# Performance work log

Measured on AMD Instinct MI355X. Metric: run time of the kernel, lower is better.

The kernel has to match this reference:

```python
import jax, jax.numpy as jnp
import numpy as np

jax.config.update("jax_enable_x64", True)  # original uses complex128 FFTs

MS_H, MS_W, MS_D = 10, 10, 2
EPS = 1e-08


def _window_mean(x, wx, wy, wz):
    """Mean over all (wx,wy,wz) VALID windows of 3D x, via a summed-area table.
    Equivalent math to tf.nn.avg_pool3d(stride 1, VALID)."""
    X, Y, Z = x.shape
    A, B, C = X - wx + 1, Y - wy + 1, Z - wz + 1  # (2*MS_W+1, 2*MS_H+1, 2*MS_D+1)
    S = jnp.pad(jnp.cumsum(jnp.cumsum(jnp.cumsum(x, 0), 1), 2), ((1, 0), (1, 0), (1, 0)))
    g = lambda ox, oy, oz: jax.lax.dynamic_slice(S, (ox, oy, oz), (A, B, C))
    ws = (g(wx, wy, wz) - g(0, wy, wz) - g(wx, 0, wz) - g(wx, wy, 0)
          + g(0, 0, wz) + g(0, wy, 0) + g(wx, 0, 0) - g(0, 0, 0))
    return ws / float(wx * wy * wz)


def _forward(fr, template):
    # fr: (1, X, Y, Z, 1) float32; template: (X, Y, Z, 1) float32
    tpl = template[..., 0]                       # (X, Y, Z)
    X, Y, Z = tpl.shape
    # --- normalize_template ---
    tpl_zm = tpl - jnp.mean(tpl)
    tpl_var = jnp.sum(jnp.square(tpl_zm)) + EPS  # scalar
    target_freq = jnp.fft.fftn(tpl_zm.astype(jnp.complex128), axes=(0, 1, 2))
    # --- normalize_image ---
    img = fr[0, ..., 0]                          # (X, Y, Z)
    imgs_zm = img - jnp.mean(img)
    wx, wy, wz = X - 2 * MS_W, Y - 2 * MS_H, Z - 2 * MS_D
    m1 = _window_mean(img, wx, wy, wz)           # avg_pool3d of img
    m2 = _window_mean(jnp.square(img), wx, wy, wz)
    shp_prod = float(X * Y * Z)
    imgs_var = m2 - jnp.square(m1) / shp_prod + EPS
    imgs_var = jnp.where(imgs_var < 0, jnp.zeros_like(imgs_var), imgs_var)
    denominator = jnp.sqrt(tpl_var * imgs_var)   # (21, 21, 5)
    # --- FFT cross-correlation ---
    fr_freq = jnp.fft.fftn(imgs_zm.astype(jnp.complex128), axes=(0, 1, 2))
    cc = jnp.abs(jnp.fft.ifftn(fr_freq * jnp.conj(target_freq), axes=(0, 1, 2))).astype(jnp.float32)
    mx, my, mz = X // 2, Y // 2, Z // 2
    rolled_cc = jnp.roll(cc, (mx, my, mz), axis=(0, 1, 2))
    ncc = rolled_cc[mx - MS_W:mx + MS_W + 1,
                    my - MS_H:my + MS_H + 1,
                    mz - MS_D:mz + MS_D + 1] / denominator.astype(jnp.float32)
    ncc = jnp.where(jnp.isnan(ncc), jnp.zeros_like(ncc), ncc)
    # --- argmax_3d + Gaussian subpixel refine ---
    A, B, C = ncc.shape
    flat_idx = jnp.argmax(ncc.reshape(-1))
    sx = flat_idx // (B * C)
    sy = (flat_idx % (B * C)) // C
    sz = flat_idx - sx * (B * C) - C * sy
    ncc_log = jnp.log(ncc)
    v = lambda dx, dy, dz: ncc_log[sx + dx, sy + dy, sz + dz]
    six = 6.0 * v(0, 0, 0)
    sh_x = (-(sx - MS_H)).astype(jnp.float32) - (v(-1, 0, 0) - v(1, 0, 0)) / (2 * v(-1, 0, 0) - six + 2 * v(1, 0, 0))
    sh_y = (-(sy - MS_W)).astype(jnp.float32) - (v(0, -1, 0) - v(0, 1, 0)) / (2 * v(0, -1, 0) - six + 2 * v(0, 1, 0))
    sh_z = (-(sz - MS_D)).astype(jnp.float32) - (v(0, 0, -1) - v(0, 0, 1)) / (2 * v(0, 0, -1) - six + 2 * v(0, 0, 1))
    return (sh_x.reshape(1, 1), sh_y.reshape(1, 1), sh_z.reshape(1, 1),
            rolled_cc[None, ..., None], ncc[None, ..., None])


def setup_inputs() -> dict:
    key = jax.random.key(0)
    k1, k2 = jax.random.split(key)
    X, Y, Z = 512, 512, 32
    base = jax.random.normal(k1, (X, Y, Z), dtype=jnp.float32)
    # box-smooth so the NCC has a broad positive peak (log-interp stays finite)
    sm = base
    for ax in range(3):
        sm = sum(jnp.roll(sm, s, ax) for s in (-2, -1, 0, 1, 2)) / 5.0
    template = sm[..., None]
    fr = (jnp.roll(sm, (3, -2, 1), axis=(0, 1, 2))
          + 0.02 * jax.random.normal(k2, (X, Y, Z), dtype=jnp.float32))[None, ..., None]
    return {"fr": fr, "template": template}


def reference(fr, template):
    return _forward(fr, template)
```

## Files before the change

### kernel.cpp

```cpp
#include <hip/hip_runtime.h>
#include <hip/hip_bf16.h>
#include <math.h>


#define NTOT 8388608
#define NLINES 262144
#define OUT_ROLL_OFF 3
#define OUT_NCC_OFF 8388611
#define WIN_PROD 6777792.0
#define EPSV 1e-8

#define WS_HC_OFF 0UL
#define WS_ZS1_OFF 67108864UL
#define WS_ZS2_OFF 77594624UL
#define WS_YS1_OFF 88080384UL
#define WS_YS2_OFF 88510464UL
#define WS_PART_OFF 88940544UL
#define WS_DENOM_OFF 88957952UL

typedef float2 cf;
__device__ __forceinline__ cf cfadd(cf a, cf b){ return make_float2(a.x+b.x, a.y+b.y); }
__device__ __forceinline__ cf cfsub(cf a, cf b){ return make_float2(a.x-b.x, a.y-b.y); }
__device__ __forceinline__ cf cfmul(cf a, cf b){ return make_float2(a.x*b.x-a.y*b.y, a.x*b.y+a.y*b.x); }
__device__ __forceinline__ cf cfnegi(cf a){ return make_float2(a.y, -a.x); }
__device__ __forceinline__ cf cfposi(cf a){ return make_float2(-a.y, a.x); }

#define RT2F 0.70710678118654752440f
__device__ __forceinline__ cf cw64f(cf v){ return make_float2(RT2F*(v.x+v.y), RT2F*(v.y-v.x)); }
__device__ __forceinline__ cf cw192f(cf v){ return make_float2(RT2F*(v.y-v.x), -RT2F*(v.x+v.y)); }
__device__ __forceinline__ cf cw64i(cf v){ return make_float2(RT2F*(v.x-v.y), RT2F*(v.x+v.y)); }
__device__ __forceinline__ cf cw192i(cf v){ return make_float2(-RT2F*(v.x+v.y), RT2F*(v.x-v.y)); }

#define SKW(i) ((i) + ((i) >> 3))
#define LROW 580

template <int H>
__device__ __forceinline__ void fwd_r4(cf* ln, const cf* tw, int lane) {
    const int MUL2 = 256 / (2 * H);
#pragma unroll
    for (int g = 0; g < 2; ++g) {
        int j = lane + 64 * g;
        int t = j & (H - 1);
        int i0 = ((j & ~(H - 1)) << 2) + t;
        cf A = ln[SKW(i0)];
        cf B = ln[SKW(i0 + H)];
        cf C = ln[SKW(i0 + 2 * H)];
        cf D = ln[SKW(i0 + 3 * H)];
        cf w1 = tw[t * MUL2];
        cf w2 = make_float2(w1.x * w1.x - w1.y * w1.y, 2.0f * w1.x * w1.y);
        cf u = cfadd(A, C), v = cfadd(B, D);
        cf p = cfmul(cfsub(A, C), w1);
        cf q = cfnegi(cfmul(cfsub(B, D), w1));
        ln[SKW(i0)]         = cfadd(u, v);
        ln[SKW(i0 + H)]     = cfmul(cfsub(u, v), w2);
        ln[SKW(i0 + 2 * H)] = cfadd(p, q);
        ln[SKW(i0 + 3 * H)] = cfmul(cfsub(p, q), w2);
    }
}

template <int H>
__device__ __forceinline__ void inv_r4(cf* ln, const cf* tw, int lane) {
    const int MUL2 = 256 / (2 * H);
#pragma unroll
    for (int g = 0; g < 2; ++g) {
        int j = lane + 64 * g;
        int t = j & (H - 1);
        int i0 = ((j & ~(H - 1)) << 2) + t;
        cf A = ln[SKW(i0)];
        cf B = ln[SKW(i0 + H)];
        cf C = ln[SKW(i0 + 2 * H)];
        cf D = ln[SKW(i0 + 3 * H)];
        cf tww = tw[t * MUL2];
        cf w2 = make_float2(tww.x, -tww.y);
        cf wH = make_float2(w2.x * w2.x - w2.y * w2.y, 2.0f * w2.x * w2.y);
        cf vb = cfmul(B, wH), vd = cfmul(D, wH);
        cf a0 = cfadd(A, vb), a1 = cfsub(A, vb);
        cf c0 = cfadd(C, vd), c1 = cfsub(C, vd);
        cf t0 = cfmul(c0, w2);
        cf t1 = cfposi(cfmul(c1, w2));
        ln[SKW(i0)]         = cfadd(a0, t0);
        ln[SKW(i0 + 2 * H)] = cfsub(a0, t0);
        ln[SKW(i0 + H)]     = cfadd(a1, t1);
        ln[SKW(i0 + 3 * H)] = cfsub(a1, t1);
    }
}

__device__ __forceinline__ void fwd_r8(cf* ln, int lane) {
    cf* rp = ln + 9 * lane;
    cf L0 = rp[0], L1 = rp[1], L2 = rp[2], L3 = rp[3];
    cf L4 = rp[4], L5 = rp[5], L6 = rp[6], L7 = rp[7];
    cf s0 = cfadd(L0, L4), d0 = cfsub(L0, L4);
    cf s1 = cfadd(L1, L5), d1 = cw64f(cfsub(L1, L5));
    cf s2 = cfadd(L2, L6), d2 = cfnegi(cfsub(L2, L6));
    cf s3 = cfadd(L3, L7), d3 = cw192f(cfsub(L3, L7));
    cf e0 = cfadd(s0, s2), e2 = cfsub(s0, s2);
    cf e1 = cfadd(s1, s3), e3 = cfnegi(cfsub(s1, s3));
    cf f0 = cfadd(d0, d2), f2 = cfsub(d0, d2);
    cf f1 = cfadd(d1, d3), f3 = cfnegi(cfsub(d1, d3));
    rp[0] = cfadd(e0, e1); rp[1] = cfsub(e0, e1);
    rp[2] = cfadd(e2, e3); rp[3] = cfsub(e2, e3);
    rp[4] = cfadd(f0, f1); rp[5] = cfsub(f0, f1);
    rp[6] = cfadd(f2, f3); rp[7] = cfsub(f2, f3);
}

__device__ __forceinline__ void inv_r8(cf* ln, int lane) {
    cf* rp = ln + 9 * lane;
    cf L0 = rp[0], L1 = rp[1], L2 = rp[2], L3 = rp[3];
    cf L4 = rp[4], L5 = rp[5], L6 = rp[6], L7 = rp[7];
    cf a0 = cfadd(L0, L1), a1 = cfsub(L0, L1), a2 = cfadd(L2, L3), a3 = cfsub(L2, L3);
    cf a4 = cfadd(L4, L5), a5 = cfsub(L4, L5), a6 = cfadd(L6, L7), a7 = cfsub(L6, L7);
    cf b0 = cfadd(a0, a2), b2 = cfsub(a0, a2);
    cf v13 = cfposi(a3);
    cf b1 = cfadd(a1, v13), b3 = cfsub(a1, v13);
    cf b4 = cfadd(a4, a6), b6 = cfsub(a4, a6);
    cf v57 = cfposi(a7);
    cf b5 = cfadd(a5, v57), b7 = cfsub(a5, v57);
    cf v0 = b4, v1 = cw64i(b5), v2 = cfposi(b6), v3 = cw192i(b7);
    rp[0] = cfadd(b0, v0); rp[4] = cfsub(b0, v0);
    rp[1] = cfadd(b1, v1); rp[5] = cfsub(b1, v1);
    rp[2] = cfadd(b2, v2); rp[6] = cfsub(b2, v2);
    rp[3] = cfadd(b3, v3); rp[7] = cfsub(b3, v3);
}

template <int INV>
__device__ __forceinline__ void line_fft512(cf* ln, const cf* tw, int lane) {
    if (!INV) {
        fwd_r4<128>(ln, tw, lane);
        __builtin_amdgcn_wave_barrier();
        fwd_r4<32>(ln, tw, lane);
        __builtin_amdgcn_wave_barrier();
        fwd_r4<8>(ln, tw, lane);
        __builtin_amdgcn_wave_barrier();
        fwd_r8(ln, lane);
    } else {
        inv_r8(ln, lane);
        __builtin_amdgcn_wave_barrier();
        inv_r4<8>(ln, tw, lane);
        __builtin_amdgcn_wave_barrier();
        inv_r4<32>(ln, tw, lane);
        __builtin_amdgcn_wave_barrier();
        inv_r4<128>(ln, tw, lane);
    }
}

static constexpr float W32CF_[16] = {
    1.0f, 0.980785280403230449f, 0.923879532511286756f, 0.831469612302545237f,
    0.707106781186547524f, 0.555570233019602225f, 0.382683432365089772f, 0.195090322016128268f,
    0.0f, -0.195090322016128268f, -0.382683432365089772f, -0.555570233019602225f,
    -0.707106781186547524f, -0.831469612302545237f, -0.923879532511286756f, -0.980785280403230449f};
static constexpr float W32SF_[16] = {
    0.0f, 0.195090322016128268f, 0.382683432365089772f, 0.555570233019602225f,
    0.707106781186547524f, 0.831469612302545237f, 0.923879532511286756f, 0.980785280403230449f,
    1.0f, 0.980785280403230449f, 0.923879532511286756f, 0.831469612302545237f,
    0.707106781186547524f, 0.555570233019602225f, 0.382683432365089772f, 0.195090322016128268f};

template <int INV>
__device__ __forceinline__ void fft32(cf* a) {
    if (INV == 0) {
#pragma unroll
        for (int s = 0; s < 5; ++s) {
            const int h = 16 >> s;
#pragma unroll
            for (int j = 0; j < 16; ++j) {
                const int t = j & (h - 1);
                const int i0 = ((j >> (4 - s)) << (5 - s)) + t;
                const int i1 = i0 + h;
                cf u = a[i0], v = a[i1];
                a[i0] = make_float2(u.x + v.x, u.y + v.y);
                float dx = u.x - v.x, dy = u.y - v.y;
                const float wc = W32CF_[t << s];
                const float ws = -W32SF_[t << s];
                a[i1] = make_float2(dx * wc - dy * ws, dx * ws + dy * wc);
            }
        }
    } else {
#pragma unroll
        for (int s = 0; s < 5; ++s) {
            const int h = 1 << s;
#pragma unroll
            for (int j = 0; j < 16; ++j) {
                const int t = j & (h - 1);
                const int i0 = ((j >> s) << (s + 1)) + t;
                const int i1 = i0 + h;
                const float wc = W32CF_[t << (4 - s)];
                const float ws = W32SF_[t << (4 - s)];
                cf u = a[i0], vr = a[i1];
                cf v = make_float2(vr.x * wc - vr.y * ws, vr.x * ws + vr.y * wc);
                a[i0] = make_float2(u.x + v.x, u.y + v.y);
                a[i1] = make_float2(u.x - v.x, u.y - v.y);
            }
        }
    }
}

__device__ __forceinline__ int mir_br(int b) {
    if (b == 0) return 0;
    int s = 31 - __clz(b);
    return (3 << s) - 1 - b;
}

__global__ __launch_bounds__(256) void k_pack_stats(const float* __restrict__ img,
                                                    const float* __restrict__ tpl,
                                                    cf* __restrict__ d,
                                                    double* __restrict__ zs1,
                                                    double* __restrict__ zs2,
                                                    double2* __restrict__ part) {
    int line = blockIdx.x * blockDim.x + threadIdx.x;
    long b = (long)line << 5;
    cf a[32];
    const float4* pi4 = (const float4*)(img + b);
    const float4* pt4 = (const float4*)(tpl + b);
#pragma unroll
    for (int q = 0; q < 8; ++q) {
        float4 fi = pi4[q];
        float4 ft = pt4[q];
        a[q * 4 + 0] = make_float2(fi.x, ft.x);
        a[q * 4 + 1] = make_float2(fi.y, ft.y);
        a[q * 4 + 2] = make_float2(fi.z, ft.z);
        a[q * 4 + 3] = make_float2(fi.w, ft.w);
    }
    {
        double s1 = 0, s2 = 0;
#pragma unroll
        for (int z = 0; z < 28; ++z) {
            double t = (double)a[z].x;
            s1 += t; s2 += t * t;
        }
        long ob = (long)line * 5;
        zs1[ob] = s1; zs2[ob] = s2;
#pragma unroll
        for (int k = 1; k <= 4; ++k) {
            double ad = (double)a[27 + k].x, r = (double)a[k - 1].x;
            s1 += ad - r;
            s2 += ad * ad - r * r;
            zs1[ob + k] = s1; zs2[ob + k] = s2;
        }
    }
    {
        double st = 0, st2 = 0;
#pragma unroll
        for (int z = 0; z < 32; ++z) {
            double t = (double)a[z].y;
            st += t; st2 += t * t;
        }
        __shared__ double r1[256], r2[256];
        int tid = threadIdx.x;
        r1[tid] = st; r2[tid] = st2;
        __syncthreads();
        for (int s = 128; s > 0; s >>= 1) {
            if (tid < s) { r1[tid] += r1[tid + s]; r2[tid] += r2[tid + s]; }
            __syncthreads();
        }
        if (tid == 0) part[blockIdx.x] = make_double2(r1[0], r2[0]);
    }
    fft32<0>(a);
#pragma unroll
    for (int z = 0; z < 32; ++z) d[b + z] = a[z];
}

__global__ __launch_bounds__(256) void k_winy(const double* __restrict__ zs1,
                                              const double* __restrict__ zs2,
                                              double* __restrict__ ys1,
                                              double* __restrict__ ys2) {
    int t = blockIdx.x * blockDim.x + threadIdx.x;
    if (t >= 2560) return;
    int x = t / 5, c = t % 5;
    long base = (long)x * 512 * 5 + c;
    double s1 = 0, s2 = 0;
    for (int y = 0; y < 492; ++y) {
        s1 += zs1[base + (long)y * 5];
        s2 += zs2[base + (long)y * 5];
    }
    long ob = (long)x * 105 + c;
    ys1[ob] = s1; ys2[ob] = s2;
    for (int k = 1; k <= 20; ++k) {
        s1 += zs1[base + (long)(491 + k) * 5] - zs1[base + (long)(k - 1) * 5];
        s2 += zs2[base + (long)(491 + k) * 5] - zs2[base + (long)(k - 1) * 5];
        ys1[ob + (long)k * 5] = s1;
        ys2[ob + (long)k * 5] = s2;
    }
}

__global__ __launch_bounds__(256) void k_winx_denom(const double* __restrict__ ys1,
                                                    const double* __restrict__ ys2,
                                                    const double2* __restrict__ part,
                                                    float* __restrict__ denom) {
    __shared__ double s1s[256], s2s[256];
    __shared__ double tplvar_s;
    int tid = threadIdx.x;
    {
        double a1 = 0, a2 = 0;
#pragma unroll
        for (int q = 0; q < 4; ++q) {
            double2 p = part[tid + 256 * q];
            a1 += p.x; a2 += p.y;
        }
        s1s[tid] = a1; s2s[tid] = a2;
        __syncthreads();
        for (int s = 128; s > 0; s >>= 1) {
            if (tid < s) { s1s[tid] += s1s[tid + s]; s2s[tid] += s2s[tid + s]; }
            __syncthreads();
        }
        if (tid == 0) {
            double S1 = s1s[0], S2 = s2s[0];
            double mu = S1 / (double)NTOT;
            tplvar_s = S2 - (double)NTOT * mu * mu + EPSV;
        }
        __syncthreads();
    }
    if (tid >= 105) return;
    const double tpl_var = tplvar_s;
    double s1 = 0, s2 = 0;
    for (int x = 0; x < 492; ++x) {
        s1 += ys1[(long)x * 105 + tid];
        s2 += ys2[(long)x * 105 + tid];
    }
    const double wm = 1.0 / WIN_PROD;
    for (int a = 0; a < 21; ++a) {
        double m1 = s1 * wm, m2 = s2 * wm;
        double iv = m2 - (m1 * m1) / (double)NTOT + EPSV;
        if (iv < 0) iv = 0;
        denom[a * 105 + tid] = (float)sqrt(tpl_var * iv);
        if (a < 20) {
            s1 += ys1[(long)(492 + a) * 105 + tid] - ys1[(long)a * 105 + tid];
            s2 += ys2[(long)(492 + a) * 105 + tid] - ys2[(long)a * 105 + tid];
        }
    }
}

template <int INV>
__global__ __launch_bounds__(1024, 8) void k_fft16(cf* __restrict__ d) {
    __shared__ cf ln[16][LROW];
    __shared__ cf tw[256];
    const int tid = threadIdx.x;
    if (tid < 256) {
        double sv, cv;
        sincos(6.283185307179586476925286766559 * (double)tid / 512.0, &sv, &cv);
        tw[tid] = make_float2((float)cv, (float)(-sv));
    }
    const long base = (long)(blockIdx.x >> 1) * 16384 + (blockIdx.x & 1) * 16;
#pragma unroll
    for (int i = 0; i < 8; ++i) {
        int idx = tid + 1024 * i;
        int lz = idx & 15, e = idx >> 4;
        ln[lz][SKW(e)] = d[base + (long)e * 32 + lz];
    }
    __syncthreads();
    const int c = tid >> 6, lane = tid & 63;
    line_fft512<INV>(ln[c], tw, lane);
    __syncthreads();
#pragma unroll
    for (int i = 0; i < 8; ++i) {
        int idx = tid + 1024 * i;
        int lz = idx & 15, e = idx >> 4;
        d[base + (long)e * 32 + lz] = ln[lz][SKW(e)];
    }
}

__global__ __launch_bounds__(1024, 4) void k_fftx_cross(cf* __restrict__ d) {
    const int bid = blockIdx.x;
    const int y = bid >> 1, tile = bid & 1;
    const int my = mir_br(y);
    if (y > my) return;
    const bool dup = (y == my);

    __shared__ cf ln[32][LROW];
    __shared__ cf tw[256];
    const int tid = threadIdx.x;
    if (tid < 256) {
        double sv, cv;
        sincos(6.283185307179586476925286766559 * (double)tid / 512.0, &sv, &cv);
        tw[tid] = make_float2((float)cv, (float)(-sv));
    }
    const int baseA = y * 32 + tile * 16;
    const int baseB = my * 32 + tile * 16;
#pragma unroll
    for (int i = 0; i < 16; ++i) {
        int idx = tid + 1024 * i;
        int lz = idx & 15, half = (idx >> 4) & 1, bx = idx >> 5;
        ln[half * 16 + lz][SKW(bx)] = d[(long)bx * 16384 + (half ? baseB : baseA) + lz];
    }
    __syncthreads();
    const int c = tid >> 6, lane = tid & 63;
    line_fft512<0>(ln[c], tw, lane);
    line_fft512<0>(ln[16 + c], tw, lane);
    __syncthreads();
    const bool dcblk = (bid == 0);
#pragma unroll
    for (int i = 0; i < 8; ++i) {
        int p = tid + 1024 * i;
        int a = p >> 9, bx = p & 511;
        int am = (tile == 0) ? mir_br(a) : 15 - a;
        int mbx = mir_br(bx);
        if (dcblk && p == 0) {
            ln[0][0] = make_float2(0.f, 0.f);
            ln[16][0] = make_float2(0.f, 0.f);
            continue;
        }
        cf h1 = ln[a][SKW(bx)];
        cf h2 = ln[16 + am][SKW(mbx)];
        float Fr = 0.5f * (h1.x + h2.x), Fi = 0.5f * (h1.y - h2.y);
        float Gr = 0.5f * (h1.y + h2.y), Gi = 0.5f * (h2.x - h1.x);
        float Pr = Fr * Gr + Fi * Gi;
        float Pi = Fi * Gr - Fr * Gi;
        ln[a][SKW(bx)] = make_float2(Pr, Pi);
        ln[16 + am][SKW(mbx)] = make_float2(Pr, -Pi);
    }
    __syncthreads();
    line_fft512<1>(ln[c], tw, lane);
    line_fft512<1>(ln[16 + c], tw, lane);
    __syncthreads();
#pragma unroll
    for (int i = 0; i < 16; ++i) {
        int idx = tid + 1024 * i;
        int lz = idx & 15, half = (idx >> 4) & 1, bx = idx >> 5;
        if (dup && half) continue;
        d[(long)bx * 16384 + (half ? baseB : baseA) + lz] = ln[half * 16 + lz][SKW(bx)];
    }
}

__global__ __launch_bounds__(256) void k_invz_abs_roll(const cf* __restrict__ d,
                                                       float* __restrict__ out) {
    int line = blockIdx.x * blockDim.x + threadIdx.x;
    int x = line >> 9, y = line & 511;
    long b = (long)line << 5;
    cf a[32];
    const float4* p4 = (const float4*)(d + b);
#pragma unroll
    for (int q = 0; q < 16; ++q) {
        float4 f = p4[q];
        a[2 * q]     = make_float2(f.x, f.y);
        a[2 * q + 1] = make_float2(f.z, f.w);
    }
    fft32<1>(a);
    const float invN = 1.0f / 8388608.0f;
    int xo = (x + 256) & 511, yo = (y + 256) & 511;
    long ob = OUT_ROLL_OFF + ((long)(xo << 9 | yo) << 5);
#pragma unroll
    for (int q = 0; q < 8; ++q) {
        int z = q * 4;
        int zo = (z + 16) & 31;
        float4 w;
        w.x = sqrtf(a[z + 0].x * a[z + 0].x + a[z + 0].y * a[z + 0].y) * invN;
        w.y = sqrtf(a[z + 1].x * a[z + 1].x + a[z + 1].y * a[z + 1].y) * invN;
        w.z = sqrtf(a[z + 2].x * a[z + 2].x + a[z + 2].y * a[z + 2].y) * invN;
        w.w = sqrtf(a[z + 3].x * a[z + 3].x + a[z + 3].y * a[z + 3].y) * invN;
        *(float4*)(out + ob + zo) = w;
    }
}

__global__ __launch_bounds__(256) void k_ncc_argmax(const float* __restrict__ denom,
                                                    float* __restrict__ out) {
    __shared__ float sncc[2205];
    __shared__ float bv[256];
    __shared__ int bi[256];
    const int tid = threadIdx.x;
    float best = -INFINITY;
    int bidx = 0x7fffffff;
    for (int i = tid; i < 2205; i += 256) {
        int a = i / 105, r = i % 105;
        int bq = r / 5, cq = r % 5;
        long ridx = OUT_ROLL_OFF + ((long)((246 + a) * 512 + (246 + bq)) << 5) + (14 + cq);
        float v = out[ridx] / denom[i];
        if (isnan(v)) v = 0.f;
        out[OUT_NCC_OFF + i] = v;
        sncc[i] = v;
        if (v > best) { best = v; bidx = i; }
    }
    bv[tid] = best;
    bi[tid] = bidx;
    __syncthreads();
    for (int s = 128; s > 0; s >>= 1) {
        if (tid < s) {
            if (bv[tid + s] > bv[tid] || (bv[tid + s] == bv[tid] && bi[tid + s] < bi[tid])) {
                bv[tid] = bv[tid + s];
                bi[tid] = bi[tid + s];
            }
        }
        __syncthreads();
    }
    if (tid == 0) {
        int idx = bi[0];
        int sx = idx / 105, sy = (idx % 105) / 5, sz = idx % 5;
        auto cl = [](int v, int n) { return v < 0 ? 0 : (v >= n ? n - 1 : v); };
        auto V = [&](int dx, int dy, int dz) {
            return logf(sncc[cl(sx + dx, 21) * 105 + cl(sy + dy, 21) * 5 + cl(sz + dz, 5)]);
        };
        float v0 = V(0, 0, 0);
        float six = 6.0f * v0;
        float am = V(-1, 0, 0), ap = V(1, 0, 0);
        float bm = V(0, -1, 0), bp = V(0, 1, 0);
        float cm = V(0, 0, -1), cp = V(0, 0, 1);
        out[0] = (float)(-(sx - 10)) - (am - ap) / (2.f * am - six + 2.f * ap);
        out[1] = (float)(-(sy - 10)) - (bm - bp) / (2.f * bm - six + 2.f * bp);
        out[2] = (float)(-(sz - 2)) - (cm - cp) / (2.f * cm - six + 2.f * cp);
    }
}

extern "C" void kernel_launch(void* const* d_in, const int* in_sizes, int n_in,
                              void* d_out, int out_size, void* d_ws, size_t ws_size,
                              hipStream_t stream) {
    const float* fr = (const float*)d_in[0];
    const float* tpl = (const float*)d_in[1];
    float* out = (float*)d_out;
    char* ws = (char*)d_ws;

    cf* Hc = (cf*)(ws + WS_HC_OFF);
    double* zs1 = (double*)(ws + WS_ZS1_OFF);
    double* zs2 = (double*)(ws + WS_ZS2_OFF);
    double* ys1 = (double*)(ws + WS_YS1_OFF);
    double* ys2 = (double*)(ws + WS_YS2_OFF);
    double2* part = (double2*)(ws + WS_PART_OFF);
    float* denom = (float*)(ws + WS_DENOM_OFF);

    k_pack_stats<<<NLINES / 256, 256, 0, stream>>>(fr, tpl, Hc, zs1, zs2, part);

    k_winy<<<10, 256, 0, stream>>>(zs1, zs2, ys1, ys2);
    k_winx_denom<<<1, 256, 0, stream>>>(ys1, ys2, part, denom);

    k_fft16<0><<<1024, 1024, 0, stream>>>(Hc);

    k_fftx_cross<<<1024, 1024, 0, stream>>>(Hc);

    k_fft16<1><<<1024, 1024, 0, stream>>>(Hc);
    k_invz_abs_roll<<<NLINES / 256, 256, 0, stream>>>(Hc, out);

    k_ncc_argmax<<<1, 256, 0, stream>>>(denom, out);
}
```

Baseline: 392.9 us.

## Use radix-8 passes in 512-point line FFT and split cross kernel into quarter tiles

Replaces the three radix-4 shared-memory passes of each 512-point line FFT with two radix-8 passes plus the final radix-8, cutting the number of LDS round trips and wave barriers per line. The x-direction cross-correlation kernel now handles 8-column quarter tiles instead of 16-column halves, with a new tile-pairing rule for the conjugate mirror. Each block therefore processes one line pair per wave instead of two, halving shared memory per block and doubling the block count to raise occupancy. Radix-8 passes need more registers per thread, and the tile pairing logic must stay correct for the mirrored tiles.

New measurement: 367.7 us. -6.4%, faster.

```diff
diff --git a/kernel.cpp b/kernel.cpp
--- a/kernel.cpp
+++ b/kernel.cpp
@@ -35,54 +35,74 @@
 #define LROW 580
 
 template <int H>
-__device__ __forceinline__ void fwd_r4(cf* ln, const cf* tw, int lane) {
-    const int MUL2 = 256 / (2 * H);
-#pragma unroll
-    for (int g = 0; g < 2; ++g) {
-        int j = lane + 64 * g;
-        int t = j & (H - 1);
-        int i0 = ((j & ~(H - 1)) << 2) + t;
-        cf A = ln[SKW(i0)];
-        cf B = ln[SKW(i0 + H)];
-        cf C = ln[SKW(i0 + 2 * H)];
-        cf D = ln[SKW(i0 + 3 * H)];
-        cf w1 = tw[t * MUL2];
-        cf w2 = make_float2(w1.x * w1.x - w1.y * w1.y, 2.0f * w1.x * w1.y);
-        cf u = cfadd(A, C), v = cfadd(B, D);
-        cf p = cfmul(cfsub(A, C), w1);
-        cf q = cfnegi(cfmul(cfsub(B, D), w1));
-        ln[SKW(i0)]         = cfadd(u, v);
-        ln[SKW(i0 + H)]     = cfmul(cfsub(u, v), w2);
-        ln[SKW(i0 + 2 * H)] = cfadd(p, q);
-        ln[SKW(i0 + 3 * H)] = cfmul(cfsub(p, q), w2);
-    }
+__device__ __forceinline__ void fwd_r8p(cf* ln, const cf* tw, int lane) {
+    const int t = lane & (H - 1);
+    const int i0 = ((lane & ~(H - 1)) << 3) + t;
+    cf x0 = ln[SKW(i0)];
+    cf x1 = ln[SKW(i0 + H)];
+    cf x2 = ln[SKW(i0 + 2 * H)];
+    cf x3 = ln[SKW(i0 + 3 * H)];
+    cf x4 = ln[SKW(i0 + 4 * H)];
+    cf x5 = ln[SKW(i0 + 5 * H)];
+    cf x6 = ln[SKW(i0 + 6 * H)];
+    cf x7 = ln[SKW(i0 + 7 * H)];
+    cf w  = tw[t * (64 / H)];
+    cf w2 = cfmul(w, w);
+    cf w4 = cfmul(w2, w2);
+    cf s0 = cfadd(x0, x4), d0 = cfmul(cfsub(x0, x4), w);
+    cf s1 = cfadd(x1, x5), d1 = cfmul(cw64f(cfsub(x1, x5)), w);
+    cf s2 = cfadd(x2, x6), d2 = cfmul(cfnegi(cfsub(x2, x6)), w);
+    cf s3 = cfadd(x3, x7), d3 = cfmul(cw192f(cfsub(x3, x7)), w);
+    cf e0 = cfadd(s0, s2), E0 = cfmul(cfsub(s0, s2), w2);
+    cf e1 = cfadd(s1, s3), E1 = cfmul(cfnegi(cfsub(s1, s3)), w2);
+    cf f0 = cfadd(d0, d2), F0 = cfmul(cfsub(d0, d2), w2);
+    cf f1 = cfadd(d1, d3), F1 = cfmul(cfnegi(cfsub(d1, d3)), w2);
+    ln[SKW(i0)]         = cfadd(e0, e1);
+    ln[SKW(i0 + H)]     = cfmul(cfsub(e0, e1), w4);
+    ln[SKW(i0 + 2 * H)] = cfadd(E0, E1);
+    ln[SKW(i0 + 3 * H)] = cfmul(cfsub(E0, E1), w4);
+    ln[SKW(i0 + 4 * H)] = cfadd(f0, f1);
+    ln[SKW(i0 + 5 * H)] = cfmul(cfsub(f0, f1), w4);
+    ln[SKW(i0 + 6 * H)] = cfadd(F0, F1);
+    ln[SKW(i0 + 7 * H)] = cfmul(cfsub(F0, F1), w4);
 }
 
 template <int H>
-__device__ __forceinline__ void inv_r4(cf* ln, const cf* tw, int lane) {
-    const int MUL2 = 256 / (2 * H);
-#pragma unroll
-    for (int g = 0; g < 2; ++g) {
-        int j = lane + 64 * g;
-        int t = j & (H - 1);
-        int i0 = ((j & ~(H - 1)) << 2) + t;
-        cf A = ln[SKW(i0)];
-        cf B = ln[SKW(i0 + H)];
-        cf C = ln[SKW(i0 + 2 * H)];
-        cf D = ln[SKW(i0 + 3 * H)];
-        cf tww = tw[t * MUL2];
-        cf w2 = make_float2(tww.x, -tww.y);
-        cf wH = make_float2(w2.x * w2.x - w2.y * w2.y, 2.0f * w2.x * w2.y);
-        cf vb = cfmul(B, wH), vd = cfmul(D, wH);
-        cf a0 = cfadd(A, vb), a1 = cfsub(A, vb);
-        cf c0 = cfadd(C, vd), c1 = cfsub(C, vd);
-        cf t0 = cfmul(c0, w2);
-        cf t1 = cfposi(cfmul(c1, w2));
-        ln[SKW(i0)]         = cfadd(a0, t0);
-        ln[SKW(i0 + 2 * H)] = cfsub(a0, t0);
-        ln[SKW(i0 + H)]     = cfadd(a1, t1);
-        ln[SKW(i0 + 3 * H)] = cfsub(a1, t1);
-    }
+__device__ __forceinline__ void inv_r8p(cf* ln, const cf* tw, int lane) {
+    const int t = lane & (H - 1);
+    const int i0 = ((lane & ~(H - 1)) << 3) + t;
+    cf x0 = ln[SKW(i0)];
+    cf x1 = ln[SKW(i0 + H)];
+    cf x2 = ln[SKW(i0 + 2 * H)];
+    cf x3 = ln[SKW(i0 + 3 * H)];
+    cf x4 = ln[SKW(i0 + 4 * H)];
+    cf x5 = ln[SKW(i0 + 5 * H)];
+    cf x6 = ln[SKW(i0 + 6 * H)];
+    cf x7 = ln[SKW(i0 + 7 * H)];
+    cf wf = tw[t * (64 / H)];
+    cf w  = make_float2(wf.x, -wf.y);
+    cf w2 = cfmul(w, w);
+    cf w4 = cfmul(w2, w2);
+    cf t1 = cfmul(x1, w4); cf a0 = cfadd(x0, t1), a1 = cfsub(x0, t1);
+    cf t3 = cfmul(x3, w4); cf a2 = cfadd(x2, t3), a3 = cfsub(x2, t3);
+    cf t5 = cfmul(x5, w4); cf a4 = cfadd(x4, t5), a5 = cfsub(x4, t5);
+    cf t7 = cfmul(x7, w4); cf a6 = cfadd(x6, t7), a7 = cfsub(x6, t7);
+    cf u2 = cfmul(a2, w2);         cf b0 = cfadd(a0, u2), b2 = cfsub(a0, u2);
+    cf u3 = cfposi(cfmul(a3, w2)); cf b1 = cfadd(a1, u3), b3 = cfsub(a1, u3);
+    cf u6 = cfmul(a6, w2);         cf b4 = cfadd(a4, u6), b6 = cfsub(a4, u6);
+    cf u7 = cfposi(cfmul(a7, w2)); cf b5 = cfadd(a5, u7), b7 = cfsub(a5, u7);
+    cf v0 = cfmul(b4, w);
+    cf v1 = cfmul(cw64i(b5), w);
+    cf v2 = cfmul(cfposi(b6), w);
+    cf v3 = cfmul(cw192i(b7), w);
+    ln[SKW(i0)]         = cfadd(b0, v0);
+    ln[SKW(i0 + 4 * H)] = cfsub(b0, v0);
+    ln[SKW(i0 + H)]     = cfadd(b1, v1);
+    ln[SKW(i0 + 5 * H)] = cfsub(b1, v1);
+    ln[SKW(i0 + 2 * H)] = cfadd(b2, v2);
+    ln[SKW(i0 + 6 * H)] = cfsub(b2, v2);
+    ln[SKW(i0 + 3 * H)] = cfadd(b3, v3);
+    ln[SKW(i0 + 7 * H)] = cfsub(b3, v3);
 }
 
 __device__ __forceinline__ void fwd_r8(cf* ln, int lane) {
@@ -125,21 +145,17 @@
 template <int INV>
 __device__ __forceinline__ void line_fft512(cf* ln, const cf* tw, int lane) {
     if (!INV) {
-        fwd_r4<128>(ln, tw, lane);
+        fwd_r8p<64>(ln, tw, lane);
         __builtin_amdgcn_wave_barrier();
-        fwd_r4<32>(ln, tw, lane);
-        __builtin_amdgcn_wave_barrier();
-        fwd_r4<8>(ln, tw, lane);
+        fwd_r8p<8>(ln, tw, lane);
         __builtin_amdgcn_wave_barrier();
         fwd_r8(ln, lane);
     } else {
         inv_r8(ln, lane);
         __builtin_amdgcn_wave_barrier();
-        inv_r4<8>(ln, tw, lane);
+        inv_r8p<8>(ln, tw, lane);
         __builtin_amdgcn_wave_barrier();
-        inv_r4<32>(ln, tw, lane);
-        __builtin_amdgcn_wave_barrier();
-        inv_r4<128>(ln, tw, lane);
+        inv_r8p<64>(ln, tw, lane);
     }
 }
 
@@ -359,12 +375,14 @@
 
 __global__ __launch_bounds__(1024, 4) void k_fftx_cross(cf* __restrict__ d) {
     const int bid = blockIdx.x;
-    const int y = bid >> 1, tile = bid & 1;
+    const int y = bid >> 2, tA = bid & 3;
     const int my = mir_br(y);
-    if (y > my) return;
-    const bool dup = (y == my);
-
-    __shared__ cf ln[32][LROW];
+    const int tB = tA ^ (tA >> 1);
+    const int keyA = (y << 2) | tA, keyB = (my << 2) | tB;
+    if (keyA > keyB) return;
+    const bool dup = (keyA == keyB);
+
+    __shared__ cf ln[16][LROW];
     __shared__ cf tw[256];
     const int tid = threadIdx.x;
     if (tid < 256) {
@@ -372,50 +390,48 @@
         sincos(6.283185307179586476925286766559 * (double)tid / 512.0, &sv, &cv);
         tw[tid] = make_float2((float)cv, (float)(-sv));
     }
-    const int baseA = y * 32 + tile * 16;
-    const int baseB = my * 32 + tile * 16;
-#pragma unroll
-    for (int i = 0; i < 16; ++i) {
+    const int baseA = y * 32 + tA * 8;
+    const int baseB = my * 32 + tB * 8;
+#pragma unroll
+    for (int i = 0; i < 8; ++i) {
         int idx = tid + 1024 * i;
-        int lz = idx & 15, half = (idx >> 4) & 1, bx = idx >> 5;
-        ln[half * 16 + lz][SKW(bx)] = d[(long)bx * 16384 + (half ? baseB : baseA) + lz];
+        int a = idx & 7, half = (idx >> 3) & 1, bx = idx >> 4;
+        ln[half * 8 + a][SKW(bx)] = d[(long)bx * 16384 + (half ? baseB : baseA) + a];
     }
     __syncthreads();
     const int c = tid >> 6, lane = tid & 63;
     line_fft512<0>(ln[c], tw, lane);
-    line_fft512<0>(ln[16 + c], tw, lane);
     __syncthreads();
     const bool dcblk = (bid == 0);
 #pragma unroll
-    for (int i = 0; i < 8; ++i) {
+    for (int i = 0; i < 4; ++i) {
         int p = tid + 1024 * i;
         int a = p >> 9, bx = p & 511;
-        int am = (tile == 0) ? mir_br(a) : 15 - a;
+        int am = (tA == 0) ? mir_br(a) : 7 - a;
         int mbx = mir_br(bx);
         if (dcblk && p == 0) {
             ln[0][0] = make_float2(0.f, 0.f);
-            ln[16][0] = make_float2(0.f, 0.f);
+            ln[8][0] = make_float2(0.f, 0.f);
             continue;
         }
         cf h1 = ln[a][SKW(bx)];
-        cf h2 = ln[16 + am][SKW(mbx)];
+        cf h2 = ln[8 + am][SKW(mbx)];
         float Fr = 0.5f * (h1.x + h2.x), Fi = 0.5f * (h1.y - h2.y);
         float Gr = 0.5f * (h1.y + h2.y), Gi = 0.5f * (h2.x - h1.x);
         float Pr = Fr * Gr + Fi * Gi;
         float Pi = Fi * Gr - Fr * Gi;
         ln[a][SKW(bx)] = make_float2(Pr, Pi);
-        ln[16 + am][SKW(mbx)] = make_float2(Pr, -Pi);
+        ln[8 + am][SKW(mbx)] = make_float2(Pr, -Pi);
     }
     __syncthreads();
     line_fft512<1>(ln[c], tw, lane);
-    line_fft512<1>(ln[16 + c], tw, lane);
-    __syncthreads();
-#pragma unroll
-    for (int i = 0; i < 16; ++i) {
+    __syncthreads();
+#pragma unroll
+    for (int i = 0; i < 8; ++i) {
         int idx = tid + 1024 * i;
-        int lz = idx & 15, half = (idx >> 4) & 1, bx = idx >> 5;
+        int a = idx & 7, half = (idx >> 3) & 1, bx = idx >> 4;
         if (dup && half) continue;
-        d[(long)bx * 16384 + (half ? baseB : baseA) + lz] = ln[half * 16 + lz][SKW(bx)];
+        d[(long)bx * 16384 + (half ? baseB : baseA) + a] = ln[half * 8 + a][SKW(bx)];
     }
 }
 
@@ -520,7 +536,7 @@
 
     k_fft16<0><<<1024, 1024, 0, stream>>>(Hc);
 
-    k_fftx_cross<<<1024, 1024, 0, stream>>>(Hc);
+    k_fftx_cross<<<2048, 1024, 0, stream>>>(Hc);
 
     k_fft16<1><<<1024, 1024, 0, stream>>>(Hc);
     k_invz_abs_roll<<<NLINES / 256, 256, 0, stream>>>(Hc, out);
```
